# Optimization experiments

Measured on AMD Instinct MI355X. Metric: run time of the kernel, lower is better.

## Reference

```python
import jax, jax.numpy as jnp
from jax import lax
import numpy as np

H = 256  # hidden_size


def gru_last(x, Wih, Whh, bih, bhh):
    """Single-layer torch-convention GRU; returns last hidden state.
    x: [B, T, C] -> [B, H]"""
    B, T, _ = x.shape
    h_dim = Whh.shape[1]
    xW = x @ Wih.T + bih  # [B, T, 3H], precompute input gates
    def step(h, xw):
        gi_r, gi_z, gi_n = jnp.split(xw, 3, axis=-1)
        gh = h @ Whh.T + bhh
        gh_r, gh_z, gh_n = jnp.split(gh, 3, axis=-1)
        r = jax.nn.sigmoid(gi_r + gh_r)
        z = jax.nn.sigmoid(gi_z + gh_z)
        n = jnp.tanh(gi_n + r * gh_n)
        return (1.0 - z) * n + z * h, None
    h0 = jnp.zeros((B, h_dim), x.dtype)
    hT, _ = lax.scan(step, h0, jnp.swapaxes(xW, 0, 1))
    return hT


def setup_inputs() -> dict:
    key = jax.random.key(0)
    ks = jax.random.split(key, 16)
    B, N, M, C, C1 = 32, 64, 64, 64, 16
    inter = 2 * H + 6 * C + C1  # 912
    s = 0.05
    x1 = jax.random.normal(ks[0], (B, N, C1), jnp.float32)
    states = jax.random.normal(ks[1], (B, N, M, C), jnp.float32)
    perm1 = jax.vmap(lambda k: jax.random.permutation(k, M))(jax.random.split(ks[2], N)).astype(jnp.int64)
    perm2 = jax.vmap(lambda k: jax.random.permutation(k, N))(jax.random.split(ks[3], N)).astype(jnp.int64)
    return {
        "x1": x1, "states": states, "perm1": perm1, "perm2": perm2,
        # shared 2D->1D GRU (ModuleList([gru]*2) shares parameters)
        "gru2d_Wih": jax.random.normal(ks[4], (3 * H, C), jnp.float32) * s,
        "gru2d_Whh": jax.random.normal(ks[5], (3 * H, H), jnp.float32) * s,
        "gru2d_bih": jax.random.normal(ks[6], (3 * H,), jnp.float32) * s,
        "gru2d_bhh": jax.random.normal(ks[7], (3 * H,), jnp.float32) * s,
        "gru1d_Wih": jax.random.normal(ks[8], (3 * H, inter), jnp.float32) * s,
        "gru1d_Whh": jax.random.normal(ks[9], (3 * H, H), jnp.float32) * s,
        "gru1d_bih": jax.random.normal(ks[10], (3 * H,), jnp.float32) * s,
        "gru1d_bhh": jax.random.normal(ks[11], (3 * H,), jnp.float32) * s,
        "fc1_W": jax.random.normal(ks[12], (H, 3 * inter + H), jnp.float32) * s,
        "fc1_b": jax.random.normal(ks[13], (H,), jnp.float32) * s,
        "fc2_W": jax.random.normal(ks[14], (1, H), jnp.float32) * s,
        "fc2_b": jax.random.normal(ks[15], (1,), jnp.float32) * s,
    }


def reference(x1, states, perm1, perm2,
              gru2d_Wih, gru2d_Whh, gru2d_bih, gru2d_bhh,
              gru1d_Wih, gru1d_Whh, gru1d_bih, gru1d_bhh,
              fc1_W, fc1_b, fc2_W, fc2_b):
    B, N, M, C = states.shape
    d = [states.max(1), states.mean(1), states.min(1),   # [B, M, C] each (N==M)
         states.max(2), states.mean(2), states.min(2)]   # [B, N, C] each
    idx = jnp.arange(N)[:, None]
    # g1[b,i,t,c] = states[b, i, perm1[i,t], c]
    g1 = states[:, idx, perm1, :]                         # [B, N, M, C]
    # g2[b,i,t,c] = states[b, perm2[i,t], i, c]
    g2 = states[:, perm2, idx, :]                         # [B, N, N, C]
    sd1 = gru_last(g1.reshape(B * N, M, C), gru2d_Wih, gru2d_Whh, gru2d_bih, gru2d_bhh).reshape(B, N, H)
    sd2 = gru_last(g2.reshape(B * N, N, C), gru2d_Wih, gru2d_Whh, gru2d_bih, gru2d_bhh).reshape(B, N, H)
    f = jnp.concatenate(d + [sd1, sd2], axis=2)           # [B, N, 6C + 2H]
    f = jnp.concatenate([x1, f], axis=-1)                 # [B, N, inter]
    hlast = gru_last(f, gru1d_Wih, gru1d_Whh, gru1d_bih, gru1d_bhh)  # [B, H]
    g = jnp.concatenate([f.max(1), f.mean(1), f.min(1), hlast], axis=1)
    h = jax.nn.relu(g @ fc1_W.T + fc1_b)
    out = h @ fc2_W.T + fc2_b
    return out.reshape(B)
```

## Files before the change

kernel.cpp:

```cpp
#include <hip/hip_runtime.h>
#include <cmath>

#define B_ 32
#define N_ 64
#define H_ 256
#define G3_ 768
#define INTER_ 912
#define KP_ 928
#define FCIN_ 2992

#define PADA 264
#define PADX 72

typedef __attribute__((ext_vector_type(8))) short short8;
typedef __attribute__((ext_vector_type(4))) short sshort4;
typedef __attribute__((ext_vector_type(4))) float float4v;

#define MFMA __builtin_amdgcn_mfma_f32_16x16x32_bf16

__device__ __forceinline__ float sigmoid_f(float x) {
    return __builtin_amdgcn_rcpf(1.0f + __builtin_amdgcn_exp2f(-1.44269504f * x));
}
__device__ __forceinline__ float tanh_fast(float x) {
    return 1.0f - 2.0f * __builtin_amdgcn_rcpf(1.0f + __builtin_amdgcn_exp2f(2.88539008f * x));
}
__device__ __forceinline__ unsigned f2bf_bits(float x) {
    unsigned u = __float_as_uint(x);
    return (u + 0x7fffu + ((u >> 16) & 1u)) >> 16;
}
__device__ __forceinline__ short f2bf(float x) { return (short)f2bf_bits(x); }

__global__ __launch_bounds__(256) void prep_kernel(
        const float* __restrict__ Whh2, const float* __restrict__ Wih2,
        const float* __restrict__ Whh1, const float* __restrict__ Wih1,
        const float* __restrict__ fc1W,
        short* __restrict__ Bfrag, short* __restrict__ Bfrag1,
        short* __restrict__ Bfrag1W, float* __restrict__ fc1Wt) {
    int idx = blockIdx.x * 256 + threadIdx.x;
    if (idx < 10 * 48 * 64 * 8) {
        int j = idx & 7, lane = (idx >> 3) & 63, tile = idx >> 9;
        int nt = tile % 48, kt = tile / 48;
        int n = nt * 16 + (lane & 15);
        int kb = (lane >> 4) * 8 + j;
        float v = (kt < 8) ? Whh2[n * 256 + kt * 32 + kb]
                           : Wih2[n * 64 + (kt - 8) * 32 + kb];
        Bfrag[idx] = f2bf(v);
    }
    if (idx < 8 * 48 * 64 * 8) {
        int j = idx & 7, lane = (idx >> 3) & 63, tile = idx >> 9;
        int nt = tile % 48, kt = tile / 48;
        int n = nt * 16 + (lane & 15);
        int k = kt * 32 + (lane >> 4) * 8 + j;
        Bfrag1[idx] = f2bf(Whh1[n * 256 + k]);
    }
    if (idx < 29 * 48 * 64 * 8) {
        int j = idx & 7, lane = (idx >> 3) & 63, tile = idx >> 9;
        int nt = tile % 48, kt = tile / 48;
        int n = nt * 16 + (lane & 15);
        int k = kt * 32 + (lane >> 4) * 8 + j;
        Bfrag1W[idx] = (k < INTER_) ? f2bf(Wih1[n * INTER_ + k]) : (short)0;
    }
    if (idx < FCIN_ * 256) {
        int o = idx & 255, i = idx >> 8;
        fc1Wt[idx] = fc1W[o * FCIN_ + i];
    }
}

__global__ __launch_bounds__(256) void reduce_states_kernel(
        const float* __restrict__ states, const float* __restrict__ x1,
        float* __restrict__ f) {
    const int c = threadIdx.x & 63;
    const int bj = blockIdx.x * 4 + (threadIdx.x >> 6);
    const int b = bj >> 6, j = bj & 63;
    const float* p1 = states + b * 262144 + j * 64 + c;
    const float* p2 = states + b * 262144 + j * 4096 + c;
    float mx1 = -1e30f, mn1 = 1e30f, sm1 = 0.f;
    float mx2 = -1e30f, mn2 = 1e30f, sm2 = 0.f;
    #pragma unroll 8
    for (int n = 0; n < 64; ++n) {
        float v = p1[n * 4096];
        mx1 = fmaxf(mx1, v); mn1 = fminf(mn1, v); sm1 += v;
    }
    #pragma unroll 8
    for (int m = 0; m < 64; ++m) {
        float v = p2[m * 64];
        mx2 = fmaxf(mx2, v); mn2 = fminf(mn2, v); sm2 += v;
    }
    float* fr = f + bj * INTER_;
    fr[16 + c]  = mx1;  fr[80 + c]  = sm1 * (1.f / 64.f);  fr[144 + c] = mn1;
    fr[208 + c] = mx2;  fr[272 + c] = sm2 * (1.f / 64.f);  fr[336 + c] = mn2;
    if (c < 16) fr[c] = x1[bj * 16 + c];
}

__global__ __launch_bounds__(512, 1) void gru2d_mfma(
        const float* __restrict__ states,
        const int* __restrict__ perm1, const int* __restrict__ perm2,
        const short* __restrict__ Bfrag,
        const float* __restrict__ bih, const float* __restrict__ bhh,
        float* __restrict__ f) {
    __shared__ short hA[2][16 * PADA];
    __shared__ short xA[2][16 * PADX];
    __shared__ short8 Blds[2 * 48 * 64];
    __shared__ int perms[1024];

    const int tid = threadIdx.x;
    const int lane = tid & 63;
    const int w = tid >> 6;
    const int m = lane & 15;
    const int q = lane >> 4;
    const bool sd2 = blockIdx.x >= 128;
    const int sblock = (blockIdx.x & 127) * 16;

    for (int i = tid; i < 1024; i += 512) {
        int r = i >> 6, t = i & 63;
        int qq = (sblock + r) & 63;
        perms[i] = sd2 ? perm2[qq * 64 + t] : perm1[qq * 64 + t];
    }
    for (int i = tid; i < 16 * PADA; i += 512) hA[0][i] = 0;
    {
        const uint4* src = (const uint4*)(Bfrag + 6 * 48 * 64 * 8);
        uint4* dst = (uint4*)Blds;
        #pragma unroll
        for (int rep = 0; rep < 12; ++rep)
            dst[tid + rep * 512] = src[tid + rep * 512];
    }

    const short8* Bf8 = (const short8*)Bfrag;
    short8 Bres[36];
    #pragma unroll
    for (int kt = 0; kt < 6; ++kt)
        #pragma unroll
        for (int j = 0; j < 6; ++j)
            Bres[kt * 6 + j] = Bf8[(kt * 48 + 8 * j + w) * 64 + lane];

    const int u0 = 16 * w + m;
    const int u1 = 128 + u0;
    const float br0 = bih[u0] + bhh[u0],             br1 = bih[u1] + bhh[u1];
    const float bz0 = bih[256 + u0] + bhh[256 + u0], bz1 = bih[256 + u1] + bhh[256 + u1];
    const float bnx0 = bih[512 + u0], bnx1 = bih[512 + u1];
    const float bnh0 = bhh[512 + u0], bnh1 = bhh[512 + u1];

    float4v hreg0 = {0.f, 0.f, 0.f, 0.f}, hreg1 = {0.f, 0.f, 0.f, 0.f};

    {
        #pragma unroll
        for (int half = 0; half < 2; ++half) {
            int i = tid + half * 512;
            int r = i >> 6, c = i & 63;
            int s = sblock + r, b = s >> 6, qq = s & 63;
            int p = perms[r * 64 + 0];
            int src = sd2 ? ((b * 64 + p) * 64 + qq) * 64 + c
                          : ((b * 64 + qq) * 64 + p) * 64 + c;
            xA[0][r * PADX + c] = f2bf(states[src]);
        }
    }
    __syncthreads();

    for (int t = 0; t < 64; ++t) {
        const short* hAc = hA[t & 1];
        const short* xAc = xA[t & 1];

        short8 Bx[12];
        #pragma unroll
        for (int kt = 0; kt < 2; ++kt)
            #pragma unroll
            for (int j = 0; j < 6; ++j)
                Bx[kt * 6 + j] = Bf8[((8 + kt) * 48 + 8 * j + w) * 64 + lane];

        float xg0 = 0.f, xg1 = 0.f;
        int w0 = -1, w1 = -1;
        if (t + 1 < 64) {
            #pragma unroll
            for (int half = 0; half < 2; ++half) {
                int i = tid + half * 512;
                int r = i >> 6, c = i & 63;
                int s = sblock + r, b = s >> 6, qq = s & 63;
                int p = perms[r * 64 + t + 1];
                int src = sd2 ? ((b * 64 + p) * 64 + qq) * 64 + c
                              : ((b * 64 + qq) * 64 + p) * 64 + c;
                float v = states[src];
                if (half == 0) { xg0 = v; w0 = r * PADX + c; }
                else           { xg1 = v; w1 = r * PADX + c; }
            }
        }

        float4v aR0 = {br0, br0, br0, br0},     aR1 = {br1, br1, br1, br1};
        float4v aZ0 = {bz0, bz0, bz0, bz0},     aZ1 = {bz1, bz1, bz1, bz1};
        float4v aNh0 = {bnh0, bnh0, bnh0, bnh0}, aNh1 = {bnh1, bnh1, bnh1, bnh1};
        float4v aNx0 = {bnx0, bnx0, bnx0, bnx0}, aNx1 = {bnx1, bnx1, bnx1, bnx1};

        #pragma unroll
        for (int kt = 0; kt < 6; ++kt) {
            short8 a = *(const short8*)(hAc + m * PADA + kt * 32 + q * 8);
            aR0  = MFMA(a, Bres[kt * 6 + 0], aR0, 0, 0, 0);
            aR1  = MFMA(a, Bres[kt * 6 + 1], aR1, 0, 0, 0);
            aZ0  = MFMA(a, Bres[kt * 6 + 2], aZ0, 0, 0, 0);
            aZ1  = MFMA(a, Bres[kt * 6 + 3], aZ1, 0, 0, 0);
            aNh0 = MFMA(a, Bres[kt * 6 + 4], aNh0, 0, 0, 0);
            aNh1 = MFMA(a, Bres[kt * 6 + 5], aNh1, 0, 0, 0);
        }
        #pragma unroll
        for (int kt = 0; kt < 2; ++kt) {
            short8 a = *(const short8*)(hAc + m * PADA + (6 + kt) * 32 + q * 8);
            short8 b0 = Blds[(kt * 48 + 8 * 0 + w) * 64 + lane];
            short8 b1 = Blds[(kt * 48 + 8 * 1 + w) * 64 + lane];
            short8 b2 = Blds[(kt * 48 + 8 * 2 + w) * 64 + lane];
            short8 b3 = Blds[(kt * 48 + 8 * 3 + w) * 64 + lane];
            short8 b4 = Blds[(kt * 48 + 8 * 4 + w) * 64 + lane];
            short8 b5 = Blds[(kt * 48 + 8 * 5 + w) * 64 + lane];
            aR0  = MFMA(a, b0, aR0, 0, 0, 0);
            aR1  = MFMA(a, b1, aR1, 0, 0, 0);
            aZ0  = MFMA(a, b2, aZ0, 0, 0, 0);
            aZ1  = MFMA(a, b3, aZ1, 0, 0, 0);
            aNh0 = MFMA(a, b4, aNh0, 0, 0, 0);
            aNh1 = MFMA(a, b5, aNh1, 0, 0, 0);
        }
        #pragma unroll
        for (int kt = 0; kt < 2; ++kt) {
            short8 a = *(const short8*)(xAc + m * PADX + kt * 32 + q * 8);
            aR0  = MFMA(a, Bx[kt * 6 + 0], aR0, 0, 0, 0);
            aR1  = MFMA(a, Bx[kt * 6 + 1], aR1, 0, 0, 0);
            aZ0  = MFMA(a, Bx[kt * 6 + 2], aZ0, 0, 0, 0);
            aZ1  = MFMA(a, Bx[kt * 6 + 3], aZ1, 0, 0, 0);
            aNx0 = MFMA(a, Bx[kt * 6 + 4], aNx0, 0, 0, 0);
            aNx1 = MFMA(a, Bx[kt * 6 + 5], aNx1, 0, 0, 0);
        }

        short* hAn = hA[(t + 1) & 1];
        #pragma unroll
        for (int p = 0; p < 4; ++p) {
            int row = q * 4 + p;
            float r0 = sigmoid_f(aR0[p]);
            float z0 = sigmoid_f(aZ0[p]);
            float n0 = tanh_fast(aNx0[p] + r0 * aNh0[p]);
            float h0 = n0 + z0 * (hreg0[p] - n0);
            hreg0[p] = h0;
            hAn[row * PADA + u0] = f2bf(h0);
            float r1 = sigmoid_f(aR1[p]);
            float z1 = sigmoid_f(aZ1[p]);
            float n1 = tanh_fast(aNx1[p] + r1 * aNh1[p]);
            float h1 = n1 + z1 * (hreg1[p] - n1);
            hreg1[p] = h1;
            hAn[row * PADA + u1] = f2bf(h1);
        }
        if (t + 1 < 64) {
            xA[(t + 1) & 1][w0] = f2bf(xg0);
            xA[(t + 1) & 1][w1] = f2bf(xg1);
        }
        __syncthreads();
    }

    const int off = sd2 ? 656 : 400;
    #pragma unroll
    for (int p = 0; p < 4; ++p) {
        int s = sblock + q * 4 + p;
        f[s * INTER_ + off + u0] = hreg0[p];
        f[s * INTER_ + off + u1] = hreg1[p];
    }
}

__global__ __launch_bounds__(256) void convert_f_kernel(
        const float* __restrict__ f, short* __restrict__ fbf) {
    int idx = blockIdx.x * 256 + threadIdx.x;
    int row = idx / 232;
    int c4 = (idx - row * 232) * 4;
    if (row >= 2048) return;
    sshort4 o;
    if (c4 < INTER_) {
        float4v v = *(const float4v*)(f + row * INTER_ + c4);
        o[0] = f2bf(v[0]); o[1] = f2bf(v[1]); o[2] = f2bf(v[2]); o[3] = f2bf(v[3]);
    } else {
        o[0] = 0; o[1] = 0; o[2] = 0; o[3] = 0;
    }
    *(sshort4*)(fbf + row * KP_ + c4) = o;
}

__global__ __launch_bounds__(256) void gemm_xw1_mfma(
        const short* __restrict__ fbf, const short* __restrict__ BfragW,
        const float* __restrict__ bih, float* __restrict__ xw) {
    const int tid = threadIdx.x;
    const int lane = tid & 63;
    const int w = tid >> 6;
    const int m = lane & 15;
    const int q = lane >> 4;
    const int tn = blockIdx.x;
    const int tm = blockIdx.y;
    const int rowb = tm * 64 + w * 16;
    const short8* Bf8 = (const short8*)BfragW;

    float4v acc[4];
    #pragma unroll
    for (int nn = 0; nn < 4; ++nn) {
        float b = bih[tn * 64 + nn * 16 + m];
        acc[nn][0] = b; acc[nn][1] = b; acc[nn][2] = b; acc[nn][3] = b;
    }

    const short* arow = fbf + (rowb + m) * KP_;
    short8 a_cur = *(const short8*)(arow + q * 8);
    short8 b_cur[4];
    #pragma unroll
    for (int nn = 0; nn < 4; ++nn)
        b_cur[nn] = Bf8[(tn * 4 + nn) * 64 + lane];

    for (int kt = 0; kt < 29; ++kt) {
        short8 a_nxt = a_cur;
        short8 b_nxt[4];
        if (kt + 1 < 29) {
            a_nxt = *(const short8*)(arow + (kt + 1) * 32 + q * 8);
            #pragma unroll
            for (int nn = 0; nn < 4; ++nn)
                b_nxt[nn] = Bf8[((kt + 1) * 48 + tn * 4 + nn) * 64 + lane];
        }
        #pragma unroll
        for (int nn = 0; nn < 4; ++nn)
            acc[nn] = MFMA(a_cur, b_cur[nn], acc[nn], 0, 0, 0);
        a_cur = a_nxt;
        #pragma unroll
        for (int nn = 0; nn < 4; ++nn) b_cur[nn] = b_nxt[nn];
    }

    #pragma unroll
    for (int p = 0; p < 4; ++p) {
        int row = rowb + q * 4 + p;
        #pragma unroll
        for (int nn = 0; nn < 4; ++nn)
            xw[row * G3_ + tn * 64 + nn * 16 + m] = acc[nn][p];
    }
}

__global__ __launch_bounds__(512, 1) void gru1d_mfma(
        const float* __restrict__ xw, const short* __restrict__ Bfrag1,
        const float* __restrict__ bhh, float* __restrict__ hlast) {
    __shared__ short hA[2][16 * PADA];
    __shared__ short8 Blds[2 * 48 * 64];

    const int tid = threadIdx.x;
    const int lane = tid & 63;
    const int w = tid >> 6;
    const int m = lane & 15;
    const int q = lane >> 4;
    const int sblock = blockIdx.x * 16;

    for (int i = tid; i < 16 * PADA; i += 512) hA[0][i] = 0;
    {
        const uint4* src = (const uint4*)(Bfrag1 + 6 * 48 * 64 * 8);
        uint4* dst = (uint4*)Blds;
        #pragma unroll
        for (int rep = 0; rep < 12; ++rep)
            dst[tid + rep * 512] = src[tid + rep * 512];
    }
    const short8* Bf8 = (const short8*)Bfrag1;
    short8 Bres[36];
    #pragma unroll
    for (int kt = 0; kt < 6; ++kt)
        #pragma unroll
        for (int j = 0; j < 6; ++j)
            Bres[kt * 6 + j] = Bf8[(kt * 48 + 8 * j + w) * 64 + lane];

    const int u0 = 16 * w + m;
    const int u1 = 128 + u0;
    const float br0 = bhh[u0],       br1 = bhh[u1];
    const float bz0 = bhh[256 + u0], bz1 = bhh[256 + u1];
    const float bn0 = bhh[512 + u0], bn1 = bhh[512 + u1];

    float4v hreg0 = {0.f, 0.f, 0.f, 0.f}, hreg1 = {0.f, 0.f, 0.f, 0.f};
    __syncthreads();

    for (int t = 0; t < 64; ++t) {
        const short* hAc = hA[t & 1];

        float giR0[4], giR1[4], giZ0[4], giZ1[4], giN0[4], giN1[4];
        #pragma unroll
        for (int p = 0; p < 4; ++p) {
            const float* gr = xw + ((sblock + q * 4 + p) * 64 + t) * G3_;
            giR0[p] = gr[u0];        giR1[p] = gr[u1];
            giZ0[p] = gr[256 + u0];  giZ1[p] = gr[256 + u1];
            giN0[p] = gr[512 + u0];  giN1[p] = gr[512 + u1];
        }

        float4v aR0 = {br0, br0, br0, br0}, aR1 = {br1, br1, br1, br1};
        float4v aZ0 = {bz0, bz0, bz0, bz0}, aZ1 = {bz1, bz1, bz1, bz1};
        float4v aN0 = {bn0, bn0, bn0, bn0}, aN1 = {bn1, bn1, bn1, bn1};

        #pragma unroll
        for (int kt = 0; kt < 6; ++kt) {
            short8 a = *(const short8*)(hAc + m * PADA + kt * 32 + q * 8);
            aR0 = MFMA(a, Bres[kt * 6 + 0], aR0, 0, 0, 0);
            aR1 = MFMA(a, Bres[kt * 6 + 1], aR1, 0, 0, 0);
            aZ0 = MFMA(a, Bres[kt * 6 + 2], aZ0, 0, 0, 0);
            aZ1 = MFMA(a, Bres[kt * 6 + 3], aZ1, 0, 0, 0);
            aN0 = MFMA(a, Bres[kt * 6 + 4], aN0, 0, 0, 0);
            aN1 = MFMA(a, Bres[kt * 6 + 5], aN1, 0, 0, 0);
        }
        #pragma unroll
        for (int kt = 0; kt < 2; ++kt) {
            short8 a = *(const short8*)(hAc + m * PADA + (6 + kt) * 32 + q * 8);
            short8 b0 = Blds[(kt * 48 + 8 * 0 + w) * 64 + lane];
            short8 b1 = Blds[(kt * 48 + 8 * 1 + w) * 64 + lane];
            short8 b2 = Blds[(kt * 48 + 8 * 2 + w) * 64 + lane];
            short8 b3 = Blds[(kt * 48 + 8 * 3 + w) * 64 + lane];
            short8 b4 = Blds[(kt * 48 + 8 * 4 + w) * 64 + lane];
            short8 b5 = Blds[(kt * 48 + 8 * 5 + w) * 64 + lane];
            aR0 = MFMA(a, b0, aR0, 0, 0, 0);
            aR1 = MFMA(a, b1, aR1, 0, 0, 0);
            aZ0 = MFMA(a, b2, aZ0, 0, 0, 0);
            aZ1 = MFMA(a, b3, aZ1, 0, 0, 0);
            aN0 = MFMA(a, b4, aN0, 0, 0, 0);
            aN1 = MFMA(a, b5, aN1, 0, 0, 0);
        }

        short* hAn = hA[(t + 1) & 1];
        #pragma unroll
        for (int p = 0; p < 4; ++p) {
            int row = q * 4 + p;
            float r0 = sigmoid_f(giR0[p] + aR0[p]);
            float z0 = sigmoid_f(giZ0[p] + aZ0[p]);
            float n0 = tanh_fast(giN0[p] + r0 * aN0[p]);
            float h0 = n0 + z0 * (hreg0[p] - n0);
            hreg0[p] = h0;
            hAn[row * PADA + u0] = f2bf(h0);
            float r1 = sigmoid_f(giR1[p] + aR1[p]);
            float z1 = sigmoid_f(giZ1[p] + aZ1[p]);
            float n1 = tanh_fast(giN1[p] + r1 * aN1[p]);
            float h1 = n1 + z1 * (hreg1[p] - n1);
            hreg1[p] = h1;
            hAn[row * PADA + u1] = f2bf(h1);
        }
        __syncthreads();
    }

    #pragma unroll
    for (int p = 0; p < 4; ++p) {
        int s = sblock + q * 4 + p;
        hlast[s * 256 + u0] = hreg0[p];
        hlast[s * 256 + u1] = hreg1[p];
    }
}

__global__ __launch_bounds__(256) void tail_kernel(
        const float* __restrict__ f, const float* __restrict__ hlast,
        const float* __restrict__ fc1Wt, const float* __restrict__ fc1b,
        const float* __restrict__ fc2W, const float* __restrict__ fc2b,
        float* __restrict__ out) {
    __shared__ float g_lds[FCIN_];
    __shared__ float red[256];
    const int tid = threadIdx.x;
    const int b = blockIdx.x;
    for (int i = tid; i < INTER_; i += 256) {
        float mx = -1e30f, mn = 1e30f, sm = 0.f;
        for (int t = 0; t < 64; ++t) {
            float v = f[(b * 64 + t) * INTER_ + i];
            mx = fmaxf(mx, v); mn = fminf(mn, v); sm += v;
        }
        g_lds[i] = mx;
        g_lds[INTER_ + i] = sm * (1.f / 64.f);
        g_lds[2 * INTER_ + i] = mn;
    }
    g_lds[3 * INTER_ + tid] = hlast[b * 256 + tid];
    __syncthreads();
    float acc = fc1b[tid];
    for (int i = 0; i < FCIN_; ++i)
        acc = fmaf(g_lds[i], fc1Wt[i * 256 + tid], acc);
    float hv = fmaxf(acc, 0.f);
    red[tid] = hv * fc2W[tid];
    __syncthreads();
    if (tid == 0) {
        float s = fc2b[0];
        for (int i = 0; i < 256; ++i) s += red[i];
        out[b] = s;
    }
}

extern "C" void kernel_launch(void* const* d_in, const int* in_sizes, int n_in,
                              void* d_out, int out_size, void* d_ws, size_t ws_size,
                              hipStream_t stream) {
    const float* x1     = (const float*)d_in[0];
    const float* states = (const float*)d_in[1];
    const int*   perm1  = (const int*)d_in[2];
    const int*   perm2  = (const int*)d_in[3];
    const float* Wih2   = (const float*)d_in[4];
    const float* Whh2   = (const float*)d_in[5];
    const float* bih2   = (const float*)d_in[6];
    const float* bhh2   = (const float*)d_in[7];
    const float* Wih1   = (const float*)d_in[8];
    const float* Whh1   = (const float*)d_in[9];
    const float* bih1   = (const float*)d_in[10];
    const float* bhh1   = (const float*)d_in[11];
    const float* fc1W   = (const float*)d_in[12];
    const float* fc1b   = (const float*)d_in[13];
    const float* fc2W   = (const float*)d_in[14];
    const float* fc2b   = (const float*)d_in[15];
    float* out = (float*)d_out;

    float* ws = (float*)d_ws;
    short* Bfrag   = (short*)ws;
    short* Bfrag1  = (short*)(ws + 122880);
    short* Bfrag1W = (short*)(ws + 122880 + 98304);
    float* fc1Wt   = ws + 577536;
    float* f       = fc1Wt + FCIN_ * 256;
    short* fbf     = (short*)(f + 2048 * INTER_);
    float* xw1     = f + 2048 * INTER_ + 950272;
    float* hlast   = xw1 + 2048 * G3_;

    prep_kernel<<<dim3(2992), 256, 0, stream>>>(Whh2, Wih2, Whh1, Wih1, fc1W,
                                                Bfrag, Bfrag1, Bfrag1W, fc1Wt);
    reduce_states_kernel<<<dim3(512), 256, 0, stream>>>(states, x1, f);
    gru2d_mfma<<<dim3(256), 512, 0, stream>>>(states, perm1, perm2, Bfrag,
                                              bih2, bhh2, f);
    convert_f_kernel<<<dim3(1856), 256, 0, stream>>>(f, fbf);
    gemm_xw1_mfma<<<dim3(12, 32), 256, 0, stream>>>(fbf, Bfrag1W, bih1, xw1);
    gru1d_mfma<<<dim3(2), 512, 0, stream>>>(xw1, Bfrag1, bhh1, hlast);
    tail_kernel<<<dim3(32), 256, 0, stream>>>(f, hlast, fc1Wt, fc1b, fc2W, fc2b, out);
}
```

Before: 632.6 us.

## Load GRU inputs directly into MFMA fragments and overlap tail reduction with 1D GRU

The 2D GRU kernel drops its LDS staging buffer for x. Each lane now loads its own permuted row of states straight into registers, converts to bf16 and feeds the MFMA, removing LDS writes and some sync work per step. The xw GEMM output is stored time-major so the 1D GRU reads contiguous rows. The f max/mean/min reduction moves into extra blocks of the 1D GRU launch so it runs alongside the serial recurrence, and the tail keeps only the FC with split accumulators and a wave shuffle reduction. Nontemporal loads are added in the reductions. The direct global loads now sit on the recurrence critical path without the previous one-step prefetch, so latency may be exposed.

Result: slower. 652.9 us (+3.2%).

```diff
diff --git a/kernel.cpp b/kernel.cpp
--- a/kernel.cpp
+++ b/kernel.cpp
@@ -8,9 +8,9 @@
 #define INTER_ 912
 #define KP_ 928
 #define FCIN_ 2992
+#define GRED_ 2736
 
 #define PADA 264
-#define PADX 72
 
 typedef __attribute__((ext_vector_type(8))) short short8;
 typedef __attribute__((ext_vector_type(4))) short sshort4;
@@ -78,12 +78,12 @@
     float mx2 = -1e30f, mn2 = 1e30f, sm2 = 0.f;
     #pragma unroll 8
     for (int n = 0; n < 64; ++n) {
-        float v = p1[n * 4096];
+        float v = __builtin_nontemporal_load(p1 + n * 4096);
         mx1 = fmaxf(mx1, v); mn1 = fminf(mn1, v); sm1 += v;
     }
     #pragma unroll 8
     for (int m = 0; m < 64; ++m) {
-        float v = p2[m * 64];
+        float v = __builtin_nontemporal_load(p2 + m * 64);
         mx2 = fmaxf(mx2, v); mn2 = fminf(mn2, v); sm2 += v;
     }
     float* fr = f + bj * INTER_;
@@ -99,7 +99,6 @@
         const float* __restrict__ bih, const float* __restrict__ bhh,
         float* __restrict__ f) {
     __shared__ short hA[2][16 * PADA];
-    __shared__ short xA[2][16 * PADX];
     __shared__ short8 Blds[2 * 48 * 64];
     __shared__ int perms[1024];
 
@@ -140,25 +139,17 @@
     const float bnx0 = bih[512 + u0], bnx1 = bih[512 + u1];
     const float bnh0 = bhh[512 + u0], bnh1 = bhh[512 + u1];
 
+    const int sglob = sblock + m;
+    const int bb = sglob >> 6, qq = sglob & 63;
+    const float* xbase = sd2 ? states + (size_t)bb * 262144 + qq * 64
+                             : states + (size_t)bb * 262144 + qq * 4096;
+    const int pstride = sd2 ? 4096 : 64;
+
     float4v hreg0 = {0.f, 0.f, 0.f, 0.f}, hreg1 = {0.f, 0.f, 0.f, 0.f};
-
-    {
-        #pragma unroll
-        for (int half = 0; half < 2; ++half) {
-            int i = tid + half * 512;
-            int r = i >> 6, c = i & 63;
-            int s = sblock + r, b = s >> 6, qq = s & 63;
-            int p = perms[r * 64 + 0];
-            int src = sd2 ? ((b * 64 + p) * 64 + qq) * 64 + c
-                          : ((b * 64 + qq) * 64 + p) * 64 + c;
-            xA[0][r * PADX + c] = f2bf(states[src]);
-        }
-    }
     __syncthreads();
 
     for (int t = 0; t < 64; ++t) {
         const short* hAc = hA[t & 1];
-        const short* xAc = xA[t & 1];
 
         short8 Bx[12];
         #pragma unroll
@@ -167,22 +158,12 @@
             for (int j = 0; j < 6; ++j)
                 Bx[kt * 6 + j] = Bf8[((8 + kt) * 48 + 8 * j + w) * 64 + lane];
 
-        float xg0 = 0.f, xg1 = 0.f;
-        int w0 = -1, w1 = -1;
-        if (t + 1 < 64) {
-            #pragma unroll
-            for (int half = 0; half < 2; ++half) {
-                int i = tid + half * 512;
-                int r = i >> 6, c = i & 63;
-                int s = sblock + r, b = s >> 6, qq = s & 63;
-                int p = perms[r * 64 + t + 1];
-                int src = sd2 ? ((b * 64 + p) * 64 + qq) * 64 + c
-                              : ((b * 64 + qq) * 64 + p) * 64 + c;
-                float v = states[src];
-                if (half == 0) { xg0 = v; w0 = r * PADX + c; }
-                else           { xg1 = v; w1 = r * PADX + c; }
-            }
-        }
+        const int p = perms[m * 64 + t];
+        const float* xs = xbase + p * pstride + q * 8;
+        float4v v00 = *(const float4v*)(xs);
+        float4v v01 = *(const float4v*)(xs + 4);
+        float4v v10 = *(const float4v*)(xs + 32);
+        float4v v11 = *(const float4v*)(xs + 36);
 
         float4v aR0 = {br0, br0, br0, br0},     aR1 = {br1, br1, br1, br1};
         float4v aZ0 = {bz0, bz0, bz0, bz0},     aZ1 = {bz1, bz1, bz1, bz1};
@@ -215,37 +196,44 @@
             aNh0 = MFMA(a, b4, aNh0, 0, 0, 0);
             aNh1 = MFMA(a, b5, aNh1, 0, 0, 0);
         }
-        #pragma unroll
-        for (int kt = 0; kt < 2; ++kt) {
-            short8 a = *(const short8*)(xAc + m * PADX + kt * 32 + q * 8);
-            aR0  = MFMA(a, Bx[kt * 6 + 0], aR0, 0, 0, 0);
-            aR1  = MFMA(a, Bx[kt * 6 + 1], aR1, 0, 0, 0);
-            aZ0  = MFMA(a, Bx[kt * 6 + 2], aZ0, 0, 0, 0);
-            aZ1  = MFMA(a, Bx[kt * 6 + 3], aZ1, 0, 0, 0);
-            aNx0 = MFMA(a, Bx[kt * 6 + 4], aNx0, 0, 0, 0);
-            aNx1 = MFMA(a, Bx[kt * 6 + 5], aNx1, 0, 0, 0);
-        }
+
+        short8 ax0, ax1;
+        #pragma unroll
+        for (int j = 0; j < 4; ++j) {
+            ax0[j]     = f2bf(v00[j]);
+            ax0[4 + j] = f2bf(v01[j]);
+            ax1[j]     = f2bf(v10[j]);
+            ax1[4 + j] = f2bf(v11[j]);
+        }
+        aR0  = MFMA(ax0, Bx[0], aR0, 0, 0, 0);
+        aR1  = MFMA(ax0, Bx[1], aR1, 0, 0, 0);
+        aZ0  = MFMA(ax0, Bx[2], aZ0, 0, 0, 0);
+        aZ1  = MFMA(ax0, Bx[3], aZ1, 0, 0, 0);
+        aNx0 = MFMA(ax0, Bx[4], aNx0, 0, 0, 0);
+        aNx1 = MFMA(ax0, Bx[5], aNx1, 0, 0, 0);
+        aR0  = MFMA(ax1, Bx[6], aR0, 0, 0, 0);
+        aR1  = MFMA(ax1, Bx[7], aR1, 0, 0, 0);
+        aZ0  = MFMA(ax1, Bx[8], aZ0, 0, 0, 0);
+        aZ1  = MFMA(ax1, Bx[9], aZ1, 0, 0, 0);
+        aNx0 = MFMA(ax1, Bx[10], aNx0, 0, 0, 0);
+        aNx1 = MFMA(ax1, Bx[11], aNx1, 0, 0, 0);
 
         short* hAn = hA[(t + 1) & 1];
         #pragma unroll
-        for (int p = 0; p < 4; ++p) {
-            int row = q * 4 + p;
-            float r0 = sigmoid_f(aR0[p]);
-            float z0 = sigmoid_f(aZ0[p]);
-            float n0 = tanh_fast(aNx0[p] + r0 * aNh0[p]);
-            float h0 = n0 + z0 * (hreg0[p] - n0);
-            hreg0[p] = h0;
+        for (int p2 = 0; p2 < 4; ++p2) {
+            int row = q * 4 + p2;
+            float r0 = sigmoid_f(aR0[p2]);
+            float z0 = sigmoid_f(aZ0[p2]);
+            float n0 = tanh_fast(aNx0[p2] + r0 * aNh0[p2]);
+            float h0 = n0 + z0 * (hreg0[p2] - n0);
+            hreg0[p2] = h0;
             hAn[row * PADA + u0] = f2bf(h0);
-            float r1 = sigmoid_f(aR1[p]);
-            float z1 = sigmoid_f(aZ1[p]);
-            float n1 = tanh_fast(aNx1[p] + r1 * aNh1[p]);
-            float h1 = n1 + z1 * (hreg1[p] - n1);
-            hreg1[p] = h1;
+            float r1 = sigmoid_f(aR1[p2]);
+            float z1 = sigmoid_f(aZ1[p2]);
+            float n1 = tanh_fast(aNx1[p2] + r1 * aNh1[p2]);
+            float h1 = n1 + z1 * (hreg1[p2] - n1);
+            hreg1[p2] = h1;
             hAn[row * PADA + u1] = f2bf(h1);
-        }
-        if (t + 1 < 64) {
-            xA[(t + 1) & 1][w0] = f2bf(xg0);
-            xA[(t + 1) & 1][w1] = f2bf(xg1);
         }
         __syncthreads();
     }
@@ -322,19 +310,39 @@
     #pragma unroll
     for (int p = 0; p < 4; ++p) {
         int row = rowb + q * 4 + p;
+        int seq = row >> 6, t = row & 63;
         #pragma unroll
         for (int nn = 0; nn < 4; ++nn)
-            xw[row * G3_ + tn * 64 + nn * 16 + m] = acc[nn][p];
-    }
-}
-
-__global__ __launch_bounds__(512, 1) void gru1d_mfma(
+            xw[(t * 32 + seq) * G3_ + tn * 64 + nn * 16 + m] = acc[nn][p];
+    }
+}
+
+__global__ __launch_bounds__(512, 1) void gru1d_freduce(
         const float* __restrict__ xw, const short* __restrict__ Bfrag1,
-        const float* __restrict__ bhh, float* __restrict__ hlast) {
+        const float* __restrict__ bhh, float* __restrict__ hlast,
+        const float* __restrict__ f, float* __restrict__ g) {
     __shared__ short hA[2][16 * PADA];
     __shared__ short8 Blds[2 * 48 * 64];
 
     const int tid = threadIdx.x;
+
+    if (blockIdx.x >= 2) {
+        const int b = blockIdx.x - 2;
+        for (int i = tid; i < INTER_; i += 512) {
+            const float* fp = f + (size_t)(b * 64) * INTER_ + i;
+            float mx = -1e30f, mn = 1e30f, sm = 0.f;
+            #pragma unroll 8
+            for (int t = 0; t < 64; ++t) {
+                float v = __builtin_nontemporal_load(fp + t * INTER_);
+                mx = fmaxf(mx, v); mn = fminf(mn, v); sm += v;
+            }
+            g[b * GRED_ + i] = mx;
+            g[b * GRED_ + INTER_ + i] = sm * (1.f / 64.f);
+            g[b * GRED_ + 2 * INTER_ + i] = mn;
+        }
+        return;
+    }
+
     const int lane = tid & 63;
     const int w = tid >> 6;
     const int m = lane & 15;
@@ -372,7 +380,7 @@
         float giR0[4], giR1[4], giZ0[4], giZ1[4], giN0[4], giN1[4];
         #pragma unroll
         for (int p = 0; p < 4; ++p) {
-            const float* gr = xw + ((sblock + q * 4 + p) * 64 + t) * G3_;
+            const float* gr = xw + (size_t)(t * 32 + sblock + q * 4 + p) * G3_;
             giR0[p] = gr[u0];        giR1[p] = gr[u1];
             giZ0[p] = gr[256 + u0];  giZ1[p] = gr[256 + u1];
             giN0[p] = gr[512 + u0];  giN1[p] = gr[512 + u1];
@@ -437,38 +445,36 @@
     }
 }
 
-__global__ __launch_bounds__(256) void tail_kernel(
-        const float* __restrict__ f, const float* __restrict__ hlast,
+__global__ __launch_bounds__(256) void tail_fc(
+        const float* __restrict__ g, const float* __restrict__ hlast,
         const float* __restrict__ fc1Wt, const float* __restrict__ fc1b,
         const float* __restrict__ fc2W, const float* __restrict__ fc2b,
         float* __restrict__ out) {
     __shared__ float g_lds[FCIN_];
-    __shared__ float red[256];
+    __shared__ float red[4];
     const int tid = threadIdx.x;
     const int b = blockIdx.x;
-    for (int i = tid; i < INTER_; i += 256) {
-        float mx = -1e30f, mn = 1e30f, sm = 0.f;
-        for (int t = 0; t < 64; ++t) {
-            float v = f[(b * 64 + t) * INTER_ + i];
-            mx = fmaxf(mx, v); mn = fminf(mn, v); sm += v;
-        }
-        g_lds[i] = mx;
-        g_lds[INTER_ + i] = sm * (1.f / 64.f);
-        g_lds[2 * INTER_ + i] = mn;
-    }
-    g_lds[3 * INTER_ + tid] = hlast[b * 256 + tid];
+    for (int i = tid; i < GRED_; i += 256) g_lds[i] = g[b * GRED_ + i];
+    g_lds[GRED_ + tid] = hlast[b * 256 + tid];
     __syncthreads();
-    float acc = fc1b[tid];
-    for (int i = 0; i < FCIN_; ++i)
-        acc = fmaf(g_lds[i], fc1Wt[i * 256 + tid], acc);
+
+    float a0 = 0.f, a1 = 0.f, a2 = 0.f, a3 = 0.f;
+    for (int i = 0; i < FCIN_; i += 4) {
+        a0 = fmaf(g_lds[i],     fc1Wt[(i) * 256 + tid],     a0);
+        a1 = fmaf(g_lds[i + 1], fc1Wt[(i + 1) * 256 + tid], a1);
+        a2 = fmaf(g_lds[i + 2], fc1Wt[(i + 2) * 256 + tid], a2);
+        a3 = fmaf(g_lds[i + 3], fc1Wt[(i + 3) * 256 + tid], a3);
+    }
+    float acc = ((a0 + a1) + (a2 + a3)) + fc1b[tid];
     float hv = fmaxf(acc, 0.f);
-    red[tid] = hv * fc2W[tid];
+    float part = hv * fc2W[tid];
+    #pragma unroll
+    for (int off = 32; off >= 1; off >>= 1)
+        part += __shfl_down(part, off, 64);
+    if ((tid & 63) == 0) red[tid >> 6] = part;
     __syncthreads();
-    if (tid == 0) {
-        float s = fc2b[0];
-        for (int i = 0; i < 256; ++i) s += red[i];
-        out[b] = s;
-    }
+    if (tid == 0)
+        out[b] = fc2b[0] + red[0] + red[1] + red[2] + red[3];
 }
 
 extern "C" void kernel_launch(void* const* d_in, const int* in_sizes, int n_in,
@@ -501,6 +507,7 @@
     short* fbf     = (short*)(f + 2048 * INTER_);
     float* xw1     = f + 2048 * INTER_ + 950272;
     float* hlast   = xw1 + 2048 * G3_;
+    float* g       = hlast + 8192;
 
     prep_kernel<<<dim3(2992), 256, 0, stream>>>(Whh2, Wih2, Whh1, Wih1, fc1W,
                                                 Bfrag, Bfrag1, Bfrag1W, fc1Wt);
@@ -509,6 +516,6 @@
                                               bih2, bhh2, f);
     convert_f_kernel<<<dim3(1856), 256, 0, stream>>>(f, fbf);
     gemm_xw1_mfma<<<dim3(12, 32), 256, 0, stream>>>(fbf, Bfrag1W, bih1, xw1);
-    gru1d_mfma<<<dim3(2), 512, 0, stream>>>(xw1, Bfrag1, bhh1, hlast);
-    tail_kernel<<<dim3(32), 256, 0, stream>>>(f, hlast, fc1Wt, fc1b, fc2W, fc2b, out);
-}
+    gru1d_freduce<<<dim3(34), 512, 0, stream>>>(xw1, Bfrag1, bhh1, hlast, f, g);
+    tail_fc<<<dim3(32), 256, 0, stream>>>(g, hlast, fc1Wt, fc1b, fc2W, fc2b, out);
+}
```
